# Kernel tuning notes

Measured on AMD Instinct MI355X. Metric: run time of the kernel, lower is better.

## Reference

```python
import jax, jax.numpy as jnp
import numpy as np

N = 100000
IN_DIM = 128
HID = 32
HEADS = 2
DEG = 16
NEG_SLOPE = 0.2


def setup_inputs() -> dict:
    rng = np.random.default_rng(0)
    E_rand = N * DEG
    src = np.concatenate([rng.integers(0, N, E_rand), np.arange(N)]).astype(np.int64)
    dst = np.concatenate([rng.integers(0, N, E_rand), np.arange(N)]).astype(np.int64)

    key = jax.random.key(0)
    ks = jax.random.split(key, 10)
    feat = jax.random.normal(ks[0], (N, IN_DIM), dtype=jnp.float32)
    # layer 1: in_dim -> HEADS * HID
    W1 = jax.random.normal(ks[1], (IN_DIM, HEADS * HID), dtype=jnp.float32) / np.sqrt(IN_DIM)
    al1 = jax.random.normal(ks[2], (HEADS, HID), dtype=jnp.float32) * 0.1
    ar1 = jax.random.normal(ks[3], (HEADS, HID), dtype=jnp.float32) * 0.1
    b1 = jnp.zeros((HEADS * HID,), dtype=jnp.float32)
    # layer 2: HEADS*HID -> 1 * HID
    W2 = jax.random.normal(ks[4], (HEADS * HID, HID), dtype=jnp.float32) / np.sqrt(HEADS * HID)
    al2 = jax.random.normal(ks[5], (1, HID), dtype=jnp.float32) * 0.1
    ar2 = jax.random.normal(ks[6], (1, HID), dtype=jnp.float32) * 0.1
    b2 = jnp.zeros((HID,), dtype=jnp.float32)
    return {"feat": feat, "W1": W1, "al1": al1, "ar1": ar1, "b1": b1,
            "W2": W2, "al2": al2, "ar2": ar2, "b2": b2,
            "src": jnp.asarray(src), "dst": jnp.asarray(dst)}


def gat_conv(feat, W, al, ar, b, src, dst, n_nodes, activation=True):
    # DGL GATConv: fc (no bias) -> per-head dot with attn vecs -> leaky_relu
    # edge score -> softmax over incoming edges of each dst -> scatter-add -> +bias -> relu
    H, D = al.shape
    h = (feat @ W).reshape(-1, H, D)                       # [N,H,D]
    el = jnp.einsum('nhd,hd->nh', h, al)                   # [N,H]
    er = jnp.einsum('nhd,hd->nh', h, ar)                   # [N,H]
    e = jax.nn.leaky_relu(el[src] + er[dst], NEG_SLOPE)    # [E,H]
    m = jax.ops.segment_max(e, dst, num_segments=n_nodes)  # [N,H]
    e = jnp.exp(e - jax.lax.stop_gradient(m)[dst])
    s = jax.ops.segment_sum(e, dst, num_segments=n_nodes)  # [N,H]
    a = e / s[dst]                                         # [E,H]
    msg = h[src] * a[:, :, None]                           # [E,H,D]
    out = jax.ops.segment_sum(msg, dst, num_segments=n_nodes)  # [N,H,D]
    out = out + b.reshape(1, H, D)
    return jax.nn.relu(out) if activation else out


def reference(feat, W1, al1, ar1, b1, W2, al2, ar2, b2, src, dst):
    h = gat_conv(feat, W1, al1, ar1, b1, src, dst, N)      # [N,HEADS,HID]
    h = h.reshape(h.shape[0], -1)                          # [N,HEADS*HID]
    h = gat_conv(h, W2, al2, ar2, b2, src, dst, N)         # [N,1,HID]
    return h.squeeze(1)                                    # [N,HID]
```

## Files before the change

kernel.cpp:

```cpp
#include <hip/hip_runtime.h>
#include <hip/hip_bf16.h>
#include <hip/hip_fp16.h>
#include <math.h>


constexpr int CAP  = 64;
constexpr int PAD  = 16;
constexpr int MAXB = 256;
constexpr int TILE = 2048;
constexpr int BCAP = 12288;

typedef _Float16 f16x8 __attribute__((ext_vector_type(8)));
typedef float    f32x4 __attribute__((ext_vector_type(4)));

__global__ __launch_bounds__(256)
void k_bin(const int* __restrict__ src, const int* __restrict__ dst,
           int* __restrict__ gcur, unsigned* __restrict__ binbuf, int E, int nbins)
{
    __shared__ int cnt[MAXB];
    __shared__ int base[MAXB];
    const int t = threadIdx.x;
    for (int b = t; b < nbins; b += 256) cnt[b] = 0;
    __syncthreads();
    const int e0 = blockIdx.x * TILE;
    int lo[8]; unsigned rec[8]; int bn[8];
    #pragma unroll
    for (int u = 0; u < 8; u++) {
        const int e = e0 + u * 256 + t;
        if (e < E) {
            const int d = dst[e], s = src[e];
            bn[u]  = d >> 9;
            rec[u] = ((unsigned)s << 9) | (unsigned)(d & 511);
            lo[u]  = atomicAdd(&cnt[bn[u]], 1);
        } else bn[u] = -1;
    }
    __syncthreads();
    for (int b = t; b < nbins; b += 256) {
        const int c = cnt[b];
        base[b] = c ? atomicAdd(&gcur[b], c) : 0;
    }
    __syncthreads();
    #pragma unroll
    for (int u = 0; u < 8; u++) if (bn[u] >= 0) {
        const int p = base[bn[u]] + lo[u];
        if (p < BCAP) binbuf[(long)bn[u] * BCAP + p] = rec[u];
    }
}

__global__ __launch_bounds__(256)
void k_scatter(const unsigned* __restrict__ binbuf, const int* __restrict__ gcur,
               int* __restrict__ deg, int* __restrict__ bucket, int nnodes)
{
    extern __shared__ int lds[];
    int* ldeg  = lds;
    int* lbuck = lds + 512;
    const int t = threadIdx.x, b = blockIdx.x;
    const int nb0 = b << 9;
    for (int i = t; i < 512; i += 256) ldeg[i] = 0;
    __syncthreads();
    const int cnt = min(gcur[b], BCAP);
    const unsigned* recs = binbuf + (long)b * BCAP;
    for (int i = t; i < cnt; i += 256) {
        const unsigned r = recs[i];
        const int nl  = (int)(r & 511u);
        const int pos = atomicAdd(&ldeg[nl], 1);
        if (pos < CAP) lbuck[nl * CAP + pos] = (int)(r >> 9);
    }
    __syncthreads();
    const int nv = min(512, nnodes - nb0);
    for (int i = t; i < nv; i += 256) deg[nb0 + i] = ldeg[i];
    const int tot4 = nv * (CAP / 4);
    int4* gb = (int4*)(bucket + (long)nb0 * CAP);
    const int4* lb = (const int4*)lbuck;
    for (int i = t; i < tot4; i += 256) gb[i] = lb[i];
}

__global__ void k_prew(const float* __restrict__ W, const float* __restrict__ al,
                       const float* __restrict__ ar, float* __restrict__ v)
{
    for (int i = threadIdx.x; i < 512; i += 256) {
        const int vec = i >> 7, k = i & 127;
        const int h = vec & 1;
        const float* a = (vec >> 1) ? ar : al;
        float s = 0.f;
        #pragma unroll
        for (int d = 0; d < 32; d++) s += W[k * 64 + h * 32 + d] * a[h * 32 + d];
        v[vec * 128 + k] = s;
    }
}

__global__ __launch_bounds__(256)
void k_gemm1(const float* __restrict__ x, const float* __restrict__ W,
             __half* __restrict__ h1, int nnodes)
{
    __shared__ _Float16 xs[64 * 128];
    __shared__ _Float16 Wh[128 * 64];
    const int tid = threadIdx.x;
    const int node0 = blockIdx.x * 64;

    for (int c = tid; c < 1024; c += 256) {
        const int row = c >> 4, k8 = c & 15;
        const int n = node0 + row;
        float4 v0 = make_float4(0,0,0,0), v1 = v0;
        if (n < nnodes) {
            v0 = ((const float4*)x)[(long)n * 32 + k8 * 2];
            v1 = ((const float4*)x)[(long)n * 32 + k8 * 2 + 1];
        }
        f16x8 h;
        h[0]=v0.x; h[1]=v0.y; h[2]=v0.z; h[3]=v0.w;
        h[4]=v1.x; h[5]=v1.y; h[6]=v1.z; h[7]=v1.w;
        const int off = (row * 256 + k8 * 16) ^ ((row & 7) << 4);
        *(f16x8*)((char*)xs + off) = h;
    }
    for (int c = tid; c < 1024; c += 256) {
        const int k = c >> 3, j8 = (c & 7) * 8;
        float4 v0 = ((const float4*)W)[(k * 64 + j8) >> 2];
        float4 v1 = ((const float4*)W)[((k * 64 + j8) >> 2) + 1];
        f16x8 h;
        h[0]=v0.x; h[1]=v0.y; h[2]=v0.z; h[3]=v0.w;
        h[4]=v1.x; h[5]=v1.y; h[6]=v1.z; h[7]=v1.w;
        *(f16x8*)(Wh + k * 64 + j8) = h;
    }
    __syncthreads();

    const int wv = tid >> 6, l = tid & 63;
    const int col = wv * 16 + (l & 15);
    const int g = l >> 4;
    f16x8 bfr[4];
    #pragma unroll
    for (int t = 0; t < 4; t++)
        #pragma unroll
        for (int e = 0; e < 8; e++)
            bfr[t][e] = Wh[(t * 32 + g * 8 + e) * 64 + col];

    #pragma unroll
    for (int nt = 0; nt < 4; nt++) {
        f32x4 acc = {0.f, 0.f, 0.f, 0.f};
        const int row = nt * 16 + (l & 15);
        #pragma unroll
        for (int t = 0; t < 4; t++) {
            const int off = (row * 256 + (t * 32 + g * 8) * 2) ^ ((row & 7) << 4);
            f16x8 af = *(const f16x8*)((const char*)xs + off);
            acc = __builtin_amdgcn_mfma_f32_16x16x32_f16(af, bfr[t], acc, 0, 0, 0);
        }
        #pragma unroll
        for (int r = 0; r < 4; r++) {
            const int n = node0 + nt * 16 + g * 4 + r;
            if (n < nnodes) h1[(long)n * 64 + col] = __float2half((float)acc[r]);
        }
    }
}

__global__ __launch_bounds__(256)
void k_att1(const float* __restrict__ x, const float* __restrict__ v,
            float* __restrict__ el, float* __restrict__ er, int nnodes)
{
    __shared__ float vs[512];
    for (int i = threadIdx.x; i < 512; i += 256) vs[i] = v[i];
    __syncthreads();
    const int gt = blockIdx.x * 256 + threadIdx.x;
    const int n = gt >> 4, li = gt & 15;
    if (n >= nnodes) return;
    const float4 xa = ((const float4*)x)[(long)n * 32 + li * 2];
    const float4 xb = ((const float4*)x)[(long)n * 32 + li * 2 + 1];
    float d0[4];
    #pragma unroll
    for (int vv = 0; vv < 4; vv++) {
        const float* vp = vs + vv * 128 + li * 8;
        d0[vv] = xa.x*vp[0] + xa.y*vp[1] + xa.z*vp[2] + xa.w*vp[3]
               + xb.x*vp[4] + xb.y*vp[5] + xb.z*vp[6] + xb.w*vp[7];
    }
    #pragma unroll
    for (int vv = 0; vv < 4; vv++) {
        d0[vv] += __shfl_xor(d0[vv], 1, 64);
        d0[vv] += __shfl_xor(d0[vv], 2, 64);
        d0[vv] += __shfl_xor(d0[vv], 4, 64);
        d0[vv] += __shfl_xor(d0[vv], 8, 64);
    }
    if (li == 0) {
        el[n * 2] = d0[0]; el[n * 2 + 1] = d0[1];
        er[n * 2] = d0[2]; er[n * 2 + 1] = d0[3];
    }
}

__global__ __launch_bounds__(256)
void k_agg1_gemm2(const __half* __restrict__ hbuf, const float* __restrict__ el,
                  const float* __restrict__ er, const int* __restrict__ deg,
                  const int* __restrict__ bucket, const float* __restrict__ b1,
                  const float* __restrict__ W2, const float* __restrict__ al2,
                  const float* __restrict__ ar2,
                  __half* __restrict__ h2, float* __restrict__ el2, float* __restrict__ er2,
                  int nnodes)
{
    constexpr int H = 2, OUT = 64, OUT2 = 32;
    const int w = threadIdx.x >> 6, lane = threadIdx.x & 63;
    const int n = blockIdx.x * 4 + w;
    __shared__ int   sbuf[4][CAP + PAD];
    __shared__ float wbuf[4][H][CAP + PAD];
    __shared__ float orow[4][OUT];
    if (n >= nnodes) return;

    const int dn = min(deg[n], CAP);
    for (int i = lane; i < dn; i += 64) sbuf[w][i] = bucket[(long)n * CAP + i];
    if (lane < PAD) {
        sbuf[w][dn + lane]    = 0;
        wbuf[w][0][dn + lane] = 0.f;
        wbuf[w][1][dn + lane] = 0.f;
    }

    const int h = lane >> 5, li = lane & 31;
    const float ern = er[(long)n * H + h];
    float m = -INFINITY;
    for (int i = li; i < dn; i += 32) {
        float e = el[(long)sbuf[w][i] * H + h] + ern;
        e = (e > 0.f) ? e : 0.2f * e;
        wbuf[w][h][i] = e;
        m = fmaxf(m, e);
    }
    #pragma unroll
    for (int off = 16; off; off >>= 1) m = fmaxf(m, __shfl_xor(m, off, 64));
    float s = 0.f;
    for (int i = li; i < dn; i += 32) {
        float v = __expf(wbuf[w][h][i] - m);
        wbuf[w][h][i] = v;
        s += v;
    }
    #pragma unroll
    for (int off = 16; off; off >>= 1) s += __shfl_xor(s, off, 64);
    const float invh = (s > 0.f) ? 1.f / s : 0.f;
    const float inv0 = __shfl(invh, 0, 64);
    const float inv1 = __shfl(invh, 32, 64);

    const int q  = lane >> 3;
    const int c8 = lane & 7;
    const int hh = c8 >> 2;
    const float invC = hh ? inv1 : inv0;
    float acc[8] = {0.f,0.f,0.f,0.f,0.f,0.f,0.f,0.f};
    for (int i = 0; i < dn; i += 16) {
        const int   sA = sbuf[w][i + q],       sB = sbuf[w][i + 8 + q];
        const float wA = wbuf[w][hh][i + q],   wB = wbuf[w][hh][i + 8 + q];
        union { float4 f4; __half2 h2v[4]; } uA, uB;
        uA.f4 = *(const float4*)(hbuf + (long)sA * OUT + c8 * 8);
        uB.f4 = *(const float4*)(hbuf + (long)sB * OUT + c8 * 8);
        #pragma unroll
        for (int j = 0; j < 4; j++) {
            const float2 xa = __half22float2(uA.h2v[j]);
            const float2 xb = __half22float2(uB.h2v[j]);
            acc[2*j]   = fmaf(xa.x, wA, acc[2*j]);
            acc[2*j+1] = fmaf(xa.y, wA, acc[2*j+1]);
            acc[2*j]   = fmaf(xb.x, wB, acc[2*j]);
            acc[2*j+1] = fmaf(xb.y, wB, acc[2*j+1]);
        }
    }
    #pragma unroll
    for (int j = 0; j < 8; j++) {
        acc[j] += __shfl_xor(acc[j], 8, 64);
        acc[j] += __shfl_xor(acc[j], 16, 64);
        acc[j] += __shfl_xor(acc[j], 32, 64);
    }
    if (q == 0) {
        #pragma unroll
        for (int j = 0; j < 8; j++)
            orow[w][c8 * 8 + j] = fmaxf(acc[j] * invC + b1[c8 * 8 + j], 0.f);
    }

    const int p = lane >> 5, j2 = lane & 31;
    float g = 0.f;
    #pragma unroll
    for (int k = 0; k < 32; k++)
        g = fmaf(orow[w][p * 32 + k], W2[(p * 32 + k) * OUT2 + j2], g);
    g += __shfl_xor(g, 32, 64);

    float ev = g * al2[j2], rv = g * ar2[j2];
    #pragma unroll
    for (int off = 16; off; off >>= 1) { ev += __shfl_xor(ev, off, 64); rv += __shfl_xor(rv, off, 64); }
    if (lane < 32) h2[(long)n * OUT2 + j2] = __float2half(g);
    if (lane == 0) { el2[n] = ev; er2[n] = rv; }
}

__global__ __launch_bounds__(256)
void k_agg2(const __half* __restrict__ h2, const float* __restrict__ el2,
            const float* __restrict__ er2, const int* __restrict__ deg,
            const int* __restrict__ bucket, const float* __restrict__ b2,
            float* __restrict__ out, int nnodes)
{
    constexpr int OUT2 = 32;
    const int w = threadIdx.x >> 6, lane = threadIdx.x & 63;
    const int n = blockIdx.x * 4 + w;
    __shared__ int   sbuf[4][CAP + PAD];
    __shared__ float wbuf[4][CAP + PAD];
    if (n >= nnodes) return;

    const int dn = min(deg[n], CAP);
    for (int i = lane; i < dn; i += 64) sbuf[w][i] = bucket[(long)n * CAP + i];
    if (lane < PAD) {
        sbuf[w][dn + lane] = 0;
        wbuf[w][dn + lane] = 0.f;
    }

    const float ern = er2[n];
    float m = -INFINITY;
    for (int i = lane; i < dn; i += 64) {
        float e = el2[sbuf[w][i]] + ern;
        e = (e > 0.f) ? e : 0.2f * e;
        wbuf[w][i] = e;
        m = fmaxf(m, e);
    }
    #pragma unroll
    for (int off = 32; off; off >>= 1) m = fmaxf(m, __shfl_xor(m, off, 64));
    float s = 0.f;
    for (int i = lane; i < dn; i += 64) {
        float v = __expf(wbuf[w][i] - m);
        wbuf[w][i] = v;
        s += v;
    }
    #pragma unroll
    for (int off = 32; off; off >>= 1) s += __shfl_xor(s, off, 64);
    const float inv = (s > 0.f) ? 1.f / s : 0.f;

    const int q  = lane >> 2;
    const int c8 = lane & 3;
    float acc[8] = {0.f,0.f,0.f,0.f,0.f,0.f,0.f,0.f};
    for (int i = 0; i < dn; i += 16) {
        const int   sA = sbuf[w][i + q];
        const float wA = wbuf[w][i + q];
        union { float4 f4; __half2 h2v[4]; } uA;
        uA.f4 = *(const float4*)(h2 + (long)sA * OUT2 + c8 * 8);
        #pragma unroll
        for (int j = 0; j < 4; j++) {
            const float2 xa = __half22float2(uA.h2v[j]);
            acc[2*j]   = fmaf(xa.x, wA, acc[2*j]);
            acc[2*j+1] = fmaf(xa.y, wA, acc[2*j+1]);
        }
    }
    #pragma unroll
    for (int j = 0; j < 8; j++) {
        acc[j] += __shfl_xor(acc[j], 4, 64);
        acc[j] += __shfl_xor(acc[j], 8, 64);
        acc[j] += __shfl_xor(acc[j], 16, 64);
        acc[j] += __shfl_xor(acc[j], 32, 64);
    }
    if (q == 0) {
        float r[8];
        #pragma unroll
        for (int j = 0; j < 8; j++)
            r[j] = fmaxf(acc[j] * inv + b2[c8 * 8 + j], 0.f);
        float4* po = (float4*)(out + (long)n * OUT2 + c8 * 8);
        po[0] = make_float4(r[0], r[1], r[2], r[3]);
        po[1] = make_float4(r[4], r[5], r[6], r[7]);
    }
}

extern "C" void kernel_launch(void* const* d_in, const int* in_sizes, int n_in,
                              void* d_out, int out_size, void* d_ws, size_t ws_size,
                              hipStream_t stream)
{
    const float* feat = (const float*)d_in[0];
    const float* W1   = (const float*)d_in[1];
    const float* al1  = (const float*)d_in[2];
    const float* ar1  = (const float*)d_in[3];
    const float* b1   = (const float*)d_in[4];
    const float* W2   = (const float*)d_in[5];
    const float* al2  = (const float*)d_in[6];
    const float* ar2  = (const float*)d_in[7];
    const float* b2   = (const float*)d_in[8];
    const int*   src  = (const int*)d_in[9];
    const int*   dst  = (const int*)d_in[10];

    const int N = in_sizes[0] / 128;
    const int E = in_sizes[9];
    const int NB = (N + 511) >> 9;

    char* ws = (char*)d_ws;
    size_t off = 0;
    auto alloc = [&](size_t bytes) -> void* {
        void* p = ws + off;
        off += (bytes + 255) & ~size_t(255);
        return p;
    };
    int*      gcur   = (int*)     alloc((size_t)MAXB * 4);
    unsigned* binbuf = (unsigned*)alloc((size_t)NB * BCAP * 4);
    int*      deg    = (int*)     alloc((size_t)N * 4);
    int*      bucket = (int*)     alloc((size_t)N * CAP * 4);
    __half*   h1     = (__half*)  alloc((size_t)N * 64 * 2);
    float*    el1    = (float*)   alloc((size_t)N * 2 * 4);
    float*    er1    = (float*)   alloc((size_t)N * 2 * 4);
    __half*   h2     = (__half*)  alloc((size_t)N * 32 * 2);
    float*    el2    = (float*)   alloc((size_t)N * 4);
    float*    er2    = (float*)   alloc((size_t)N * 4);
    float*    vpre   = (float*)   alloc(512 * 4);

    hipMemsetAsync(gcur, 0, (size_t)NB * 4, stream);

    k_prew<<<1, 256, 0, stream>>>(W1, al1, ar1, vpre);
    k_bin<<<(E + TILE - 1) / TILE, 256, 0, stream>>>(src, dst, gcur, binbuf, E, NB);
    k_scatter<<<NB, 256, (512 + 512 * CAP) * 4, stream>>>(binbuf, gcur, deg, bucket, N);
    k_gemm1<<<(N + 63) / 64, 256, 0, stream>>>(feat, W1, h1, N);
    k_att1<<<(N * 16 + 255) / 256, 256, 0, stream>>>(feat, vpre, el1, er1, N);
    k_agg1_gemm2<<<(N + 3) / 4, 256, 0, stream>>>(h1, el1, er1, deg, bucket, b1,
                                                  W2, al2, ar2, h2, el2, er2, N);
    k_agg2<<<(N + 3) / 4, 256, 0, stream>>>(h2, el2, er2, deg, bucket, b2,
                                            (float*)d_out, N);
}
```

Before: 309.3 us.

## Restructure GAT pipeline: fuse binning with GEMM1, MFMA attention, split GEMM2

Binning and the layer-1 GEMM now run as one horizontally fused launch. The attention logits el/er come from an extra MFMA tile using precomputed W·a vectors, which removes the separate k_att1 pass over the features. Layer-2 projection moves out of the aggregation kernel into an MFMA GEMM that also emits el2/er2. Softmax drops the max subtraction and assumes at most 64 edges, so it needs only one exp pass. Bins shrink to 256 nodes, the memset is folded into k_prew, and buffers are aliased. The risks are exp overflow without max-shift, losing edges when a bin exceeds BCAP, and an extra intermediate write of o1.

New measurement: 281.7 us. 1.1x faster.

```diff
diff --git a/kernel.cpp b/kernel.cpp
--- a/kernel.cpp
+++ b/kernel.cpp
@@ -1,114 +1,105 @@
 #include <hip/hip_runtime.h>
-#include <hip/hip_bf16.h>
 #include <hip/hip_fp16.h>
 #include <math.h>
 
 
 constexpr int CAP  = 64;
-constexpr int PAD  = 16;
-constexpr int MAXB = 256;
+constexpr int MAXB = 512;
 constexpr int TILE = 2048;
-constexpr int BCAP = 12288;
+constexpr int BCAP = 5120;
 
 typedef _Float16 f16x8 __attribute__((ext_vector_type(8)));
 typedef float    f32x4 __attribute__((ext_vector_type(4)));
 
 __global__ __launch_bounds__(256)
-void k_bin(const int* __restrict__ src, const int* __restrict__ dst,
-           int* __restrict__ gcur, unsigned* __restrict__ binbuf, int E, int nbins)
-{
-    __shared__ int cnt[MAXB];
-    __shared__ int base[MAXB];
+void k_prew(const float* __restrict__ W1, const float* __restrict__ al1, const float* __restrict__ ar1,
+            const float* __restrict__ W2, const float* __restrict__ al2, const float* __restrict__ ar2,
+            _Float16* __restrict__ vh1, _Float16* __restrict__ B2h, int* __restrict__ gcur)
+{
     const int t = threadIdx.x;
-    for (int b = t; b < nbins; b += 256) cnt[b] = 0;
-    __syncthreads();
-    const int e0 = blockIdx.x * TILE;
-    int lo[8]; unsigned rec[8]; int bn[8];
-    #pragma unroll
-    for (int u = 0; u < 8; u++) {
-        const int e = e0 + u * 256 + t;
-        if (e < E) {
-            const int d = dst[e], s = src[e];
-            bn[u]  = d >> 9;
-            rec[u] = ((unsigned)s << 9) | (unsigned)(d & 511);
-            lo[u]  = atomicAdd(&cnt[bn[u]], 1);
-        } else bn[u] = -1;
-    }
-    __syncthreads();
-    for (int b = t; b < nbins; b += 256) {
-        const int c = cnt[b];
-        base[b] = c ? atomicAdd(&gcur[b], c) : 0;
-    }
-    __syncthreads();
-    #pragma unroll
-    for (int u = 0; u < 8; u++) if (bn[u] >= 0) {
-        const int p = base[bn[u]] + lo[u];
-        if (p < BCAP) binbuf[(long)bn[u] * BCAP + p] = rec[u];
-    }
-}
-
-__global__ __launch_bounds__(256)
-void k_scatter(const unsigned* __restrict__ binbuf, const int* __restrict__ gcur,
-               int* __restrict__ deg, int* __restrict__ bucket, int nnodes)
-{
-    extern __shared__ int lds[];
-    int* ldeg  = lds;
-    int* lbuck = lds + 512;
-    const int t = threadIdx.x, b = blockIdx.x;
-    const int nb0 = b << 9;
-    for (int i = t; i < 512; i += 256) ldeg[i] = 0;
-    __syncthreads();
-    const int cnt = min(gcur[b], BCAP);
-    const unsigned* recs = binbuf + (long)b * BCAP;
-    for (int i = t; i < cnt; i += 256) {
-        const unsigned r = recs[i];
-        const int nl  = (int)(r & 511u);
-        const int pos = atomicAdd(&ldeg[nl], 1);
-        if (pos < CAP) lbuck[nl * CAP + pos] = (int)(r >> 9);
-    }
-    __syncthreads();
-    const int nv = min(512, nnodes - nb0);
-    for (int i = t; i < nv; i += 256) deg[nb0 + i] = ldeg[i];
-    const int tot4 = nv * (CAP / 4);
-    int4* gb = (int4*)(bucket + (long)nb0 * CAP);
-    const int4* lb = (const int4*)lbuck;
-    for (int i = t; i < tot4; i += 256) gb[i] = lb[i];
-}
-
-__global__ void k_prew(const float* __restrict__ W, const float* __restrict__ al,
-                       const float* __restrict__ ar, float* __restrict__ v)
-{
-    for (int i = threadIdx.x; i < 512; i += 256) {
-        const int vec = i >> 7, k = i & 127;
-        const int h = vec & 1;
-        const float* a = (vec >> 1) ? ar : al;
+    for (int i = t; i < 128 * 16; i += 256) {
+        const int k = i >> 4, c = i & 15;
         float s = 0.f;
-        #pragma unroll
-        for (int d = 0; d < 32; d++) s += W[k * 64 + h * 32 + d] * a[h * 32 + d];
-        v[vec * 128 + k] = s;
-    }
-}
-
-__global__ __launch_bounds__(256)
-void k_gemm1(const float* __restrict__ x, const float* __restrict__ W,
-             __half* __restrict__ h1, int nnodes)
-{
-    __shared__ _Float16 xs[64 * 128];
-    __shared__ _Float16 Wh[128 * 64];
+        if (c < 4) {
+            const int h = c & 1;
+            const float* a = (c >> 1) ? ar1 : al1;
+            #pragma unroll
+            for (int d = 0; d < 32; d++) s += W1[k * 64 + h * 32 + d] * a[h * 32 + d];
+        }
+        vh1[i] = (_Float16)s;
+    }
+    for (int i = t; i < 64 * 64; i += 256) {
+        const int k = i >> 6, c = i & 63;
+        float s = 0.f;
+        if (c < 32) s = W2[k * 32 + c];
+        else if (c < 34) {
+            const float* a = (c == 32) ? al2 : ar2;
+            #pragma unroll
+            for (int d = 0; d < 32; d++) s += W2[k * 32 + d] * a[d];
+        }
+        B2h[i] = (_Float16)s;
+    }
+    for (int b = t; b < MAXB; b += 256) gcur[b] = 0;
+}
+
+__global__ __launch_bounds__(256)
+void k_front(const int* __restrict__ src, const int* __restrict__ dst,
+             int* __restrict__ gcur, unsigned* __restrict__ binbuf, int E, int Gbin,
+             const float* __restrict__ x, const float* __restrict__ W,
+             const _Float16* __restrict__ vh1,
+             __half* __restrict__ h1, float* __restrict__ el, float* __restrict__ er,
+             int nnodes)
+{
+    __shared__ alignas(16) char smem[32 * 1024];
     const int tid = threadIdx.x;
-    const int node0 = blockIdx.x * 64;
+
+    if ((int)blockIdx.x < Gbin) {
+        int* cnt  = (int*)smem;
+        int* base = cnt + MAXB;
+        for (int b = tid; b < MAXB; b += 256) cnt[b] = 0;
+        __syncthreads();
+        const int e0 = blockIdx.x * TILE;
+        int lo[8]; unsigned rec[8]; int bn[8];
+        #pragma unroll
+        for (int u = 0; u < 8; u++) {
+            const int e = e0 + u * 256 + tid;
+            if (e < E) {
+                const int d = dst[e];
+                bn[u]  = d >> 8;
+                rec[u] = ((unsigned)src[e] << 8) | (unsigned)(d & 255);
+                lo[u]  = atomicAdd(&cnt[bn[u]], 1);
+            } else bn[u] = -1;
+        }
+        __syncthreads();
+        for (int b = tid; b < MAXB; b += 256) {
+            const int c = cnt[b];
+            base[b] = c ? atomicAdd(&gcur[b], c) : 0;
+        }
+        __syncthreads();
+        #pragma unroll
+        for (int u = 0; u < 8; u++) if (bn[u] >= 0) {
+            const int p = base[bn[u]] + lo[u];
+            if ((unsigned)p < (unsigned)BCAP)
+                binbuf[(long)bn[u] * BCAP + p] = rec[u];
+        }
+        return;
+    }
+
+    _Float16* xs = (_Float16*)smem;
+    _Float16* Wh = xs + 64 * 128;
+    const int node0 = ((int)blockIdx.x - Gbin) * 64;
 
     for (int c = tid; c < 1024; c += 256) {
         const int row = c >> 4, k8 = c & 15;
         const int n = node0 + row;
-        float4 v0 = make_float4(0,0,0,0), v1 = v0;
+        float4 v0 = make_float4(0, 0, 0, 0), v1 = v0;
         if (n < nnodes) {
             v0 = ((const float4*)x)[(long)n * 32 + k8 * 2];
             v1 = ((const float4*)x)[(long)n * 32 + k8 * 2 + 1];
         }
         f16x8 h;
-        h[0]=v0.x; h[1]=v0.y; h[2]=v0.z; h[3]=v0.w;
-        h[4]=v1.x; h[5]=v1.y; h[6]=v1.z; h[7]=v1.w;
+        h[0] = v0.x; h[1] = v0.y; h[2] = v0.z; h[3] = v0.w;
+        h[4] = v1.x; h[5] = v1.y; h[6] = v1.z; h[7] = v1.w;
         const int off = (row * 256 + k8 * 16) ^ ((row & 7) << 4);
         *(f16x8*)((char*)xs + off) = h;
     }
@@ -117,8 +108,8 @@
         float4 v0 = ((const float4*)W)[(k * 64 + j8) >> 2];
         float4 v1 = ((const float4*)W)[((k * 64 + j8) >> 2) + 1];
         f16x8 h;
-        h[0]=v0.x; h[1]=v0.y; h[2]=v0.z; h[3]=v0.w;
-        h[4]=v1.x; h[5]=v1.y; h[6]=v1.z; h[7]=v1.w;
+        h[0] = v0.x; h[1] = v0.y; h[2] = v0.z; h[3] = v0.w;
+        h[4] = v1.x; h[5] = v1.y; h[6] = v1.z; h[7] = v1.w;
         *(f16x8*)(Wh + k * 64 + j8) = h;
     }
     __syncthreads();
@@ -126,119 +117,115 @@
     const int wv = tid >> 6, l = tid & 63;
     const int col = wv * 16 + (l & 15);
     const int g = l >> 4;
-    f16x8 bfr[4];
+    f16x8 bfr[4], vfr[4];
     #pragma unroll
     for (int t = 0; t < 4; t++)
         #pragma unroll
         for (int e = 0; e < 8; e++)
             bfr[t][e] = Wh[(t * 32 + g * 8 + e) * 64 + col];
+    if (wv == 0) {
+        #pragma unroll
+        for (int t = 0; t < 4; t++)
+            #pragma unroll
+            for (int e = 0; e < 8; e++)
+                vfr[t][e] = vh1[(t * 32 + g * 8 + e) * 16 + (l & 15)];
+    }
 
     #pragma unroll
     for (int nt = 0; nt < 4; nt++) {
-        f32x4 acc = {0.f, 0.f, 0.f, 0.f};
+        f32x4 acc = {0.f, 0.f, 0.f, 0.f}, accv = {0.f, 0.f, 0.f, 0.f};
         const int row = nt * 16 + (l & 15);
         #pragma unroll
         for (int t = 0; t < 4; t++) {
             const int off = (row * 256 + (t * 32 + g * 8) * 2) ^ ((row & 7) << 4);
             f16x8 af = *(const f16x8*)((const char*)xs + off);
             acc = __builtin_amdgcn_mfma_f32_16x16x32_f16(af, bfr[t], acc, 0, 0, 0);
+            if (wv == 0)
+                accv = __builtin_amdgcn_mfma_f32_16x16x32_f16(af, vfr[t], accv, 0, 0, 0);
         }
         #pragma unroll
         for (int r = 0; r < 4; r++) {
             const int n = node0 + nt * 16 + g * 4 + r;
-            if (n < nnodes) h1[(long)n * 64 + col] = __float2half((float)acc[r]);
-        }
-    }
-}
-
-__global__ __launch_bounds__(256)
-void k_att1(const float* __restrict__ x, const float* __restrict__ v,
-            float* __restrict__ el, float* __restrict__ er, int nnodes)
-{
-    __shared__ float vs[512];
-    for (int i = threadIdx.x; i < 512; i += 256) vs[i] = v[i];
+            if (n < nnodes) {
+                h1[(long)n * 64 + col] = __float2half((float)acc[r]);
+                if (wv == 0) {
+                    const int c4 = l & 15;
+                    if (c4 < 2)      el[n * 2 + c4]       = (float)accv[r];
+                    else if (c4 < 4) er[n * 2 + (c4 - 2)] = (float)accv[r];
+                }
+            }
+        }
+    }
+}
+
+__global__ __launch_bounds__(256)
+void k_scatter(const unsigned* __restrict__ binbuf, const int* __restrict__ gcur,
+               int* __restrict__ deg, int* __restrict__ bucket, int nnodes)
+{
+    extern __shared__ int lds[];
+    int* ldeg  = lds;
+    int* lbuck = lds + 256;
+    const int t = threadIdx.x, b = blockIdx.x;
+    const int nb0 = b << 8;
+    ldeg[t] = 0;
     __syncthreads();
-    const int gt = blockIdx.x * 256 + threadIdx.x;
-    const int n = gt >> 4, li = gt & 15;
-    if (n >= nnodes) return;
-    const float4 xa = ((const float4*)x)[(long)n * 32 + li * 2];
-    const float4 xb = ((const float4*)x)[(long)n * 32 + li * 2 + 1];
-    float d0[4];
-    #pragma unroll
-    for (int vv = 0; vv < 4; vv++) {
-        const float* vp = vs + vv * 128 + li * 8;
-        d0[vv] = xa.x*vp[0] + xa.y*vp[1] + xa.z*vp[2] + xa.w*vp[3]
-               + xb.x*vp[4] + xb.y*vp[5] + xb.z*vp[6] + xb.w*vp[7];
-    }
-    #pragma unroll
-    for (int vv = 0; vv < 4; vv++) {
-        d0[vv] += __shfl_xor(d0[vv], 1, 64);
-        d0[vv] += __shfl_xor(d0[vv], 2, 64);
-        d0[vv] += __shfl_xor(d0[vv], 4, 64);
-        d0[vv] += __shfl_xor(d0[vv], 8, 64);
-    }
-    if (li == 0) {
-        el[n * 2] = d0[0]; el[n * 2 + 1] = d0[1];
-        er[n * 2] = d0[2]; er[n * 2 + 1] = d0[3];
-    }
-}
-
-__global__ __launch_bounds__(256)
-void k_agg1_gemm2(const __half* __restrict__ hbuf, const float* __restrict__ el,
-                  const float* __restrict__ er, const int* __restrict__ deg,
-                  const int* __restrict__ bucket, const float* __restrict__ b1,
-                  const float* __restrict__ W2, const float* __restrict__ al2,
-                  const float* __restrict__ ar2,
-                  __half* __restrict__ h2, float* __restrict__ el2, float* __restrict__ er2,
-                  int nnodes)
-{
-    constexpr int H = 2, OUT = 64, OUT2 = 32;
+    const int cnt = min(max(gcur[b], 0), BCAP);
+    const unsigned* recs = binbuf + (long)b * BCAP;
+    for (int i = t; i < cnt; i += 256) {
+        const unsigned r = recs[i];
+        const int nl  = (int)(r & 255u);
+        const int pos = atomicAdd(&ldeg[nl], 1);
+        if (pos < CAP) lbuck[nl * CAP + pos] = (int)(r >> 8);
+    }
+    __syncthreads();
+    const int nv = min(256, nnodes - nb0);
+    if (t < nv) deg[nb0 + t] = ldeg[t];
+    const int tot4 = nv * (CAP / 4);
+    int4* gb = (int4*)(bucket + (long)nb0 * CAP);
+    const int4* lb = (const int4*)lbuck;
+    for (int i = t; i < tot4; i += 256) gb[i] = lb[i];
+}
+
+__global__ __launch_bounds__(256)
+void k_agg1(const __half* __restrict__ hbuf, const float* __restrict__ el,
+            const float* __restrict__ er, const int* __restrict__ deg,
+            const int* __restrict__ bucket, const float* __restrict__ b1,
+            __half* __restrict__ o1, int nnodes)
+{
+    constexpr int OUT = 64;
     const int w = threadIdx.x >> 6, lane = threadIdx.x & 63;
     const int n = blockIdx.x * 4 + w;
-    __shared__ int   sbuf[4][CAP + PAD];
-    __shared__ float wbuf[4][H][CAP + PAD];
-    __shared__ float orow[4][OUT];
+    __shared__ int    sbuf[4][CAP];
+    __shared__ float2 wbuf[4][CAP];
     if (n >= nnodes) return;
 
     const int dn = min(deg[n], CAP);
-    for (int i = lane; i < dn; i += 64) sbuf[w][i] = bucket[(long)n * CAP + i];
-    if (lane < PAD) {
-        sbuf[w][dn + lane]    = 0;
-        wbuf[w][0][dn + lane] = 0.f;
-        wbuf[w][1][dn + lane] = 0.f;
-    }
-
-    const int h = lane >> 5, li = lane & 31;
-    const float ern = er[(long)n * H + h];
-    float m = -INFINITY;
-    for (int i = li; i < dn; i += 32) {
-        float e = el[(long)sbuf[w][i] * H + h] + ern;
-        e = (e > 0.f) ? e : 0.2f * e;
-        wbuf[w][h][i] = e;
-        m = fmaxf(m, e);
-    }
-    #pragma unroll
-    for (int off = 16; off; off >>= 1) m = fmaxf(m, __shfl_xor(m, off, 64));
-    float s = 0.f;
-    for (int i = li; i < dn; i += 32) {
-        float v = __expf(wbuf[w][h][i] - m);
-        wbuf[w][h][i] = v;
-        s += v;
-    }
-    #pragma unroll
-    for (int off = 16; off; off >>= 1) s += __shfl_xor(s, off, 64);
-    const float invh = (s > 0.f) ? 1.f / s : 0.f;
-    const float inv0 = __shfl(invh, 0, 64);
-    const float inv1 = __shfl(invh, 32, 64);
-
-    const int q  = lane >> 3;
-    const int c8 = lane & 7;
-    const int hh = c8 >> 2;
+    const int sv = (lane < dn) ? bucket[(long)n * CAP + lane] : 0;
+    sbuf[w][lane] = sv;
+
+    const float2 ernv = ((const float2*)er)[n];
+    const float2 elv  = ((const float2*)el)[sv];
+    float e0 = elv.x + ernv.x; e0 = (e0 > 0.f) ? e0 : 0.2f * e0;
+    float e1 = elv.y + ernv.y; e1 = (e1 > 0.f) ? e1 : 0.2f * e1;
+    const float w0 = (lane < dn) ? __expf(e0) : 0.f;
+    const float w1 = (lane < dn) ? __expf(e1) : 0.f;
+    wbuf[w][lane] = make_float2(w0, w1);
+    float s0 = w0, s1 = w1;
+    #pragma unroll
+    for (int off = 32; off; off >>= 1) {
+        s0 += __shfl_xor(s0, off, 64);
+        s1 += __shfl_xor(s1, off, 64);
+    }
+    const float inv0 = (s0 > 0.f) ? 1.f / s0 : 0.f;
+    const float inv1 = (s1 > 0.f) ? 1.f / s1 : 0.f;
+
+    const int q = lane >> 3, c8 = lane & 7, hh = c8 >> 2;
     const float invC = hh ? inv1 : inv0;
     float acc[8] = {0.f,0.f,0.f,0.f,0.f,0.f,0.f,0.f};
     for (int i = 0; i < dn; i += 16) {
-        const int   sA = sbuf[w][i + q],       sB = sbuf[w][i + 8 + q];
-        const float wA = wbuf[w][hh][i + q],   wB = wbuf[w][hh][i + 8 + q];
+        const int   sA = sbuf[w][i + q],                     sB = sbuf[w][i + 8 + q];
+        const float wA = ((const float*)&wbuf[w][i + q])[hh];
+        const float wB = ((const float*)&wbuf[w][i + 8 + q])[hh];
         union { float4 f4; __half2 h2v[4]; } uA, uB;
         uA.f4 = *(const float4*)(hbuf + (long)sA * OUT + c8 * 8);
         uB.f4 = *(const float4*)(hbuf + (long)sB * OUT + c8 * 8);
@@ -259,23 +246,67 @@
         acc[j] += __shfl_xor(acc[j], 32, 64);
     }
     if (q == 0) {
+        f16x8 ov;
         #pragma unroll
         for (int j = 0; j < 8; j++)
-            orow[w][c8 * 8 + j] = fmaxf(acc[j] * invC + b1[c8 * 8 + j], 0.f);
-    }
-
-    const int p = lane >> 5, j2 = lane & 31;
-    float g = 0.f;
-    #pragma unroll
-    for (int k = 0; k < 32; k++)
-        g = fmaf(orow[w][p * 32 + k], W2[(p * 32 + k) * OUT2 + j2], g);
-    g += __shfl_xor(g, 32, 64);
-
-    float ev = g * al2[j2], rv = g * ar2[j2];
-    #pragma unroll
-    for (int off = 16; off; off >>= 1) { ev += __shfl_xor(ev, off, 64); rv += __shfl_xor(rv, off, 64); }
-    if (lane < 32) h2[(long)n * OUT2 + j2] = __float2half(g);
-    if (lane == 0) { el2[n] = ev; er2[n] = rv; }
+            ov[j] = (_Float16)fmaxf(acc[j] * invC + b1[c8 * 8 + j], 0.f);
+        *(f16x8*)((char*)o1 + (long)n * 128 + c8 * 16) = ov;
+    }
+}
+
+__global__ __launch_bounds__(256)
+void k_gemm2(const __half* __restrict__ o1, const _Float16* __restrict__ B2h,
+             __half* __restrict__ h2, float* __restrict__ el2, float* __restrict__ er2,
+             int nnodes)
+{
+    __shared__ _Float16 xs[64 * 64];
+    const int tid = threadIdx.x;
+    const int node0 = blockIdx.x * 64;
+
+    for (int c = tid; c < 512; c += 256) {
+        const int row = c >> 3, k8 = c & 7;
+        const int n = node0 + row;
+        f16x8 h = {0,0,0,0,0,0,0,0};
+        if (n < nnodes) h = *(const f16x8*)((const char*)o1 + (long)n * 128 + k8 * 16);
+        const int off = (row * 128 + k8 * 16) ^ ((row & 7) << 4);
+        *(f16x8*)((char*)xs + off) = h;
+    }
+    __syncthreads();
+
+    const int wv = tid >> 6, l = tid & 63;
+    if (wv == 3) return;
+    const int col = wv * 16 + (l & 15);
+    const int g = l >> 4;
+    f16x8 bfr[2];
+    #pragma unroll
+    for (int t = 0; t < 2; t++)
+        #pragma unroll
+        for (int e = 0; e < 8; e++)
+            bfr[t][e] = B2h[(t * 32 + g * 8 + e) * 64 + col];
+
+    #pragma unroll
+    for (int nt = 0; nt < 4; nt++) {
+        f32x4 acc = {0.f, 0.f, 0.f, 0.f};
+        const int row = nt * 16 + (l & 15);
+        #pragma unroll
+        for (int t = 0; t < 2; t++) {
+            const int off = (row * 128 + (t * 32 + g * 8) * 2) ^ ((row & 7) << 4);
+            f16x8 af = *(const f16x8*)((const char*)xs + off);
+            acc = __builtin_amdgcn_mfma_f32_16x16x32_f16(af, bfr[t], acc, 0, 0, 0);
+        }
+        #pragma unroll
+        for (int r = 0; r < 4; r++) {
+            const int n = node0 + nt * 16 + g * 4 + r;
+            if (n < nnodes) {
+                if (wv < 2) h2[(long)n * 32 + col] = __float2half((float)acc[r]);
+                else {
+                    const int c4 = l & 15;
+                    if (c4 == 0)      el2[n] = (float)acc[r];
+                    else if (c4 == 1) er2[n] = (float)acc[r];
+                }
+            }
+        }
+    }
 }
 
 __global__ __launch_bounds__(256)
@@ -284,48 +315,32 @@
             const int* __restrict__ bucket, const float* __restrict__ b2,
             float* __restrict__ out, int nnodes)
 {
-    constexpr int OUT2 = 32;
     const int w = threadIdx.x >> 6, lane = threadIdx.x & 63;
     const int n = blockIdx.x * 4 + w;
-    __shared__ int   sbuf[4][CAP + PAD];
-    __shared__ float wbuf[4][CAP + PAD];
+    __shared__ int   sbuf[4][CAP];
+    __shared__ float wbuf[4][CAP];
     if (n >= nnodes) return;
 
     const int dn = min(deg[n], CAP);
-    for (int i = lane; i < dn; i += 64) sbuf[w][i] = bucket[(long)n * CAP + i];
-    if (lane < PAD) {
-        sbuf[w][dn + lane] = 0;
-        wbuf[w][dn + lane] = 0.f;
-    }
+    const int sv = (lane < dn) ? bucket[(long)n * CAP + lane] : 0;
+    sbuf[w][lane] = sv;
 
     const float ern = er2[n];
-    float m = -INFINITY;
-    for (int i = lane; i < dn; i += 64) {
-        float e = el2[sbuf[w][i]] + ern;
-        e = (e > 0.f) ? e : 0.2f * e;
-        wbuf[w][i] = e;
-        m = fmaxf(m, e);
-    }
-    #pragma unroll
-    for (int off = 32; off; off >>= 1) m = fmaxf(m, __shfl_xor(m, off, 64));
-    float s = 0.f;
-    for (int i = lane; i < dn; i += 64) {
-        float v = __expf(wbuf[w][i] - m);
-        wbuf[w][i] = v;
-        s += v;
-    }
+    float e = el2[sv] + ern; e = (e > 0.f) ? e : 0.2f * e;
+    const float wt = (lane < dn) ? __expf(e) : 0.f;
+    wbuf[w][lane] = wt;
+    float s = wt;
     #pragma unroll
     for (int off = 32; off; off >>= 1) s += __shfl_xor(s, off, 64);
     const float inv = (s > 0.f) ? 1.f / s : 0.f;
 
-    const int q  = lane >> 2;
-    const int c8 = lane & 3;
+    const int q = lane >> 2, c8 = lane & 3;
     float acc[8] = {0.f,0.f,0.f,0.f,0.f,0.f,0.f,0.f};
     for (int i = 0; i < dn; i += 16) {
         const int   sA = sbuf[w][i + q];
         const float wA = wbuf[w][i + q];
         union { float4 f4; __half2 h2v[4]; } uA;
-        uA.f4 = *(const float4*)(h2 + (long)sA * OUT2 + c8 * 8);
+        uA.f4 = *(const float4*)(h2 + (long)sA * 32 + c8 * 8);
         #pragma unroll
         for (int j = 0; j < 4; j++) {
             const float2 xa = __half22float2(uA.h2v[j]);
@@ -345,7 +360,7 @@
         #pragma unroll
         for (int j = 0; j < 8; j++)
             r[j] = fmaxf(acc[j] * inv + b2[c8 * 8 + j], 0.f);
-        float4* po = (float4*)(out + (long)n * OUT2 + c8 * 8);
+        float4* po = (float4*)(out + (long)n * 32 + c8 * 8);
         po[0] = make_float4(r[0], r[1], r[2], r[3]);
         po[1] = make_float4(r[4], r[5], r[6], r[7]);
     }
@@ -367,9 +382,9 @@
     const int*   src  = (const int*)d_in[9];
     const int*   dst  = (const int*)d_in[10];
 
-    const int N = in_sizes[0] / 128;
-    const int E = in_sizes[9];
-    const int NB = (N + 511) >> 9;
+    const int N  = in_sizes[0] / 128;
+    const int E  = in_sizes[9];
+    const int NB = (N + 255) >> 8;
 
     char* ws = (char*)d_ws;
     size_t off = 0;
@@ -378,27 +393,33 @@
         off += (bytes + 255) & ~size_t(255);
         return p;
     };
+    const size_t szA = ((size_t)NB * BCAP * 4 > (size_t)N * 64 * 2)
+                     ? (size_t)NB * BCAP * 4 : (size_t)N * 64 * 2;
+    char*     A      = (char*)    alloc(szA);
+    unsigned* binbuf = (unsigned*)A;
+    __half*   o1     = (__half*)  A;
+    char*     B      = (char*)    alloc((size_t)N * 64 * 2);
+    __half*   h1     = (__half*)  B;
+    __half*   h2     = (__half*)  B;
     int*      gcur   = (int*)     alloc((size_t)MAXB * 4);
-    unsigned* binbuf = (unsigned*)alloc((size_t)NB * BCAP * 4);
     int*      deg    = (int*)     alloc((size_t)N * 4);
     int*      bucket = (int*)     alloc((size_t)N * CAP * 4);
-    __half*   h1     = (__half*)  alloc((size_t)N * 64 * 2);
     float*    el1    = (float*)   alloc((size_t)N * 2 * 4);
     float*    er1    = (float*)   alloc((size_t)N * 2 * 4);
-    __half*   h2     = (__half*)  alloc((size_t)N * 32 * 2);
     float*    el2    = (float*)   alloc((size_t)N * 4);
     float*    er2    = (float*)   alloc((size_t)N * 4);
-    float*    vpre   = (float*)   alloc(512 * 4);
-
-    hipMemsetAsync(gcur, 0, (size_t)NB * 4, stream);
-
-    k_prew<<<1, 256, 0, stream>>>(W1, al1, ar1, vpre);
-    k_bin<<<(E + TILE - 1) / TILE, 256, 0, stream>>>(src, dst, gcur, binbuf, E, NB);
-    k_scatter<<<NB, 256, (512 + 512 * CAP) * 4, stream>>>(binbuf, gcur, deg, bucket, N);
-    k_gemm1<<<(N + 63) / 64, 256, 0, stream>>>(feat, W1, h1, N);
-    k_att1<<<(N * 16 + 255) / 256, 256, 0, stream>>>(feat, vpre, el1, er1, N);
-    k_agg1_gemm2<<<(N + 3) / 4, 256, 0, stream>>>(h1, el1, er1, deg, bucket, b1,
-                                                  W2, al2, ar2, h2, el2, er2, N);
+    _Float16* vh1    = (_Float16*)alloc(128 * 16 * 2);
+    _Float16* B2h    = (_Float16*)alloc(64 * 64 * 2);
+
+    const int Gbin  = (E + TILE - 1) / TILE;
+    const int Ggemm = (N + 63) / 64;
+
+    k_prew<<<1, 256, 0, stream>>>(W1, al1, ar1, W2, al2, ar2, vh1, B2h, gcur);
+    k_front<<<Gbin + Ggemm, 256, 0, stream>>>(src, dst, gcur, binbuf, E, Gbin,
+                                              feat, W1, vh1, h1, el1, er1, N);
+    k_scatter<<<NB, 256, (256 + 256 * CAP) * 4, stream>>>(binbuf, gcur, deg, bucket, N);
+    k_agg1<<<(N + 3) / 4, 256, 0, stream>>>(h1, el1, er1, deg, bucket, b1, o1, N);
+    k_gemm2<<<(N + 63) / 64, 256, 0, stream>>>(o1, B2h, h2, el2, er2, N);
     k_agg2<<<(N + 3) / 4, 256, 0, stream>>>(h2, el2, er2, deg, bucket, b2,
                                             (float*)d_out, N);
 }
```
